# Kernel tuning notes

Measured on AMD Instinct MI355X. Metric: run time of the kernel, lower is better.

## Reference

```python
import jax, jax.numpy as jnp
import numpy as np

N_NODES = 50000
N_EDGES = 800000
DIM_IN = 128
DIM_OUT = 64


def setup_inputs() -> dict:
    key = jax.random.key(0)
    k1, k2, k3, k4 = jax.random.split(key, 4)
    x = jax.random.normal(k1, (N_NODES, DIM_IN), dtype=jnp.float32)
    edge_index = jax.random.randint(k2, (2, N_EDGES), 0, N_NODES, dtype=jnp.int64)
    W = jax.random.normal(k3, (DIM_IN, DIM_OUT), dtype=jnp.float32) / np.sqrt(DIM_IN)
    b = jax.random.normal(k4, (DIM_OUT,), dtype=jnp.float32) * 0.01
    return {"x": x, "edge_index": edge_index, "W": W, "b": b}


def reference(x, edge_index, W, b):
    # Faithful PyG GCNConv: add self-loops, symmetric deg normalization,
    # linear transform then normalized scatter-add aggregation, then bias.
    N = x.shape[0]
    h = x @ W  # [N, dim_out] — transform before propagate (PyG order)

    loops = jnp.arange(N, dtype=edge_index.dtype)
    src = jnp.concatenate([edge_index[0], loops])  # [E+N]
    dst = jnp.concatenate([edge_index[1], loops])  # [E+N]

    ones = jnp.ones(src.shape[0], dtype=h.dtype)
    deg = jax.ops.segment_sum(ones, dst, num_segments=N)  # in-degree incl. self-loop
    dinv = jnp.where(deg > 0, jax.lax.rsqrt(deg), 0.0)
    norm = dinv[src] * dinv[dst]  # [E+N]

    msgs = h[src] * norm[:, None]  # gather + scale
    out = jax.ops.segment_sum(msgs, dst, num_segments=N) + b  # scatter-add
    return jax.nn.log_softmax(out, axis=1)
```

## Files before the change

### kernel.cpp

```cpp
#include <hip/hip_runtime.h>
#include <hip/hip_fp16.h>
#include <cstdint>
#include <cstddef>

#define N_NODES 50000
#define N_EDGES 800000
#define DIM_IN  128
#define DIM_OUT 64

#define BSHIFT  6
#define BNODES  64
#define NB      1024
#define NBK     ((N_NODES + BNODES - 1) / BNODES)
#define EB      4096
#define SORTB   ((N_EDGES + EB - 1) / EB)
#define NE4     (N_EDGES / 4)
#define CAPB    1280
#define GROWS   512
#define GEMMB   ((N_NODES + GROWS - 1) / GROWS)
#define GPAD    16

typedef _Float16 f16x8 __attribute__((ext_vector_type(8)));
typedef float    f32x4 __attribute__((ext_vector_type(4)));

__global__ __launch_bounds__(256) void k_zero(int* __restrict__ gcnt) {
    const int i = blockIdx.x * 256 + threadIdx.x;
    if (i < NB * GPAD) gcnt[i] = 0;
}

__global__ __launch_bounds__(1024) void kFG(const int* __restrict__ ei,
                                            int* __restrict__ gcnt,
                                            unsigned* __restrict__ pairs,
                                            const float* __restrict__ x,
                                            const float* __restrict__ W,
                                            __half* __restrict__ h) {
    const int t = threadIdx.x;
    if (blockIdx.x < SORTB) {
        __shared__ int hcnt[NB];
        __shared__ int cur[NB];
        const int blk = blockIdx.x;
        hcnt[t] = 0;
        __syncthreads();
        const int4* src4 = (const int4*)ei;
        const int4* dst4 = (const int4*)(ei + N_EDGES);
        const int g = blk * (EB / 4) + t;
        int4 sv, dv;
        const bool live = (g < NE4);
        if (live) {
            dv = dst4[g];
            sv = src4[g];
            atomicAdd(&hcnt[dv.x >> BSHIFT], 1);
            atomicAdd(&hcnt[dv.y >> BSHIFT], 1);
            atomicAdd(&hcnt[dv.z >> BSHIFT], 1);
            atomicAdd(&hcnt[dv.w >> BSHIFT], 1);
        }
        __syncthreads();
        {
            const int c = hcnt[t];
            const int base = c ? atomicAdd(&gcnt[t * GPAD], c) : 0;
            cur[t] = t * CAPB + base;
        }
        __syncthreads();
        if (live) {
            int b, p;
            b = dv.x >> BSHIFT; p = atomicAdd(&cur[b], 1);
            if (p < b * CAPB + CAPB) pairs[p] = ((unsigned)sv.x << 16) | (unsigned)dv.x;
            b = dv.y >> BSHIFT; p = atomicAdd(&cur[b], 1);
            if (p < b * CAPB + CAPB) pairs[p] = ((unsigned)sv.y << 16) | (unsigned)dv.y;
            b = dv.z >> BSHIFT; p = atomicAdd(&cur[b], 1);
            if (p < b * CAPB + CAPB) pairs[p] = ((unsigned)sv.z << 16) | (unsigned)dv.z;
            b = dv.w >> BSHIFT; p = atomicAdd(&cur[b], 1);
            if (p < b * CAPB + CAPB) pairs[p] = ((unsigned)sv.w << 16) | (unsigned)dv.w;
        }
    } else {
        const int u = blockIdx.x - SORTB;
        const int w = t >> 6;
        const int l = t & 63;
        const int q = l >> 4;
        const int m16 = l & 15;

        f16x8 bf[4][4];
#pragma unroll
        for (int kc = 0; kc < 4; ++kc)
#pragma unroll
            for (int ct = 0; ct < 4; ++ct) {
                const float* wp = W + (size_t)(kc * 32 + q * 8) * DIM_OUT + ct * 16 + m16;
                f16x8 v;
#pragma unroll
                for (int j = 0; j < 8; ++j) v[j] = (_Float16)wp[(size_t)j * DIM_OUT];
                bf[kc][ct] = v;
            }

        const int base = u * GROWS + w * 32;
#pragma unroll
        for (int rt = 0; rt < 2; ++rt) {
            const int m0 = base + rt * 16;
            int mrow = m0 + m16;
            if (mrow >= N_NODES) mrow = N_NODES - 1;

            f16x8 af[4];
#pragma unroll
            for (int kc = 0; kc < 4; ++kc) {
                const float4* xp = (const float4*)(x + (size_t)mrow * DIM_IN + kc * 32 + q * 8);
                const float4 p0 = xp[0], p1 = xp[1];
                f16x8 a;
                a[0] = (_Float16)p0.x; a[1] = (_Float16)p0.y;
                a[2] = (_Float16)p0.z; a[3] = (_Float16)p0.w;
                a[4] = (_Float16)p1.x; a[5] = (_Float16)p1.y;
                a[6] = (_Float16)p1.z; a[7] = (_Float16)p1.w;
                af[kc] = a;
            }

            f32x4 acc[4];
#pragma unroll
            for (int ct = 0; ct < 4; ++ct) acc[ct] = (f32x4){0.f, 0.f, 0.f, 0.f};
#pragma unroll
            for (int kc = 0; kc < 4; ++kc)
#pragma unroll
                for (int ct = 0; ct < 4; ++ct)
                    acc[ct] = __builtin_amdgcn_mfma_f32_16x16x32_f16(af[kc], bf[kc][ct], acc[ct], 0, 0, 0);

#pragma unroll
            for (int reg = 0; reg < 4; ++reg) {
                const int r = m0 + q * 4 + reg;
                if (r < N_NODES) {
#pragma unroll
                    for (int ct = 0; ct < 4; ++ct)
                        h[(size_t)r * DIM_OUT + ct * 16 + m16] = __float2half(acc[ct][reg]);
                }
            }
        }
    }
}

__global__ __launch_bounds__(256) void kScale(const unsigned* __restrict__ pairs,
                                              const int* __restrict__ gcnt,
                                              __half* __restrict__ h) {
    __shared__ int cnt[BNODES];
    __shared__ float sdinv[BNODES];
    const int b = blockIdx.x, t = threadIdx.x;
    const int eb = b * CAPB;
    const int count = min(gcnt[b * GPAD], CAPB);
    const int ee = eb + count;

    if (t < BNODES) cnt[t] = 0;
    __syncthreads();

    {
        int i = eb + t;
        for (; i + 768 < ee; i += 1024) {
            const unsigned p0 = pairs[i];
            const unsigned p1 = pairs[i + 256];
            const unsigned p2 = pairs[i + 512];
            const unsigned p3 = pairs[i + 768];
            atomicAdd(&cnt[p0 & (BNODES - 1)], 1);
            atomicAdd(&cnt[p1 & (BNODES - 1)], 1);
            atomicAdd(&cnt[p2 & (BNODES - 1)], 1);
            atomicAdd(&cnt[p3 & (BNODES - 1)], 1);
        }
        for (; i < ee; i += 256) atomicAdd(&cnt[pairs[i] & (BNODES - 1)], 1);
    }
    __syncthreads();

    if (t < BNODES) sdinv[t] = rsqrtf((float)(cnt[t] + 1));
    __syncthreads();

    f16x8* h8w = (f16x8*)h;
    for (int idx = t; idx < BNODES * 8; idx += 256) {
        const int r = idx >> 3;
        const int n = (b << BSHIFT) + r;
        if (n < N_NODES) {
            const float d = sdinv[r];
            f16x8 v = h8w[(size_t)n * 8 + (idx & 7)];
#pragma unroll
            for (int j = 0; j < 8; ++j) v[j] = (_Float16)((float)v[j] * d);
            h8w[(size_t)n * 8 + (idx & 7)] = v;
        }
    }
}

__global__ __launch_bounds__(512) void kAgg(const unsigned* __restrict__ pairs,
                                            const int* __restrict__ gcnt,
                                            const __half* __restrict__ h,
                                            const float* __restrict__ bvec,
                                            float* __restrict__ out) {
    __shared__ int cnt[BNODES];
    __shared__ int cur[BNODES];
    __shared__ float sdinv[BNODES];
    __shared__ unsigned short lcsr[CAPB];
    const int b = blockIdx.x, t = threadIdx.x;
    const int eb = b * CAPB;
    const int count = min(gcnt[b * GPAD], CAPB);
    const int ee = eb + count;

    if (t < BNODES) cnt[t] = 0;
    __syncthreads();

    {
        int i = eb + t;
        for (; i + 512 < ee; i += 1024) {
            const unsigned p0 = pairs[i];
            const unsigned p1 = pairs[i + 512];
            atomicAdd(&cnt[p0 & (BNODES - 1)], 1);
            atomicAdd(&cnt[p1 & (BNODES - 1)], 1);
        }
        for (; i < ee; i += 512) atomicAdd(&cnt[pairs[i] & (BNODES - 1)], 1);
    }
    __syncthreads();

    if (t < 64) {
        const int lane = t;
        const int v = cnt[lane];
        int xs = v;
#pragma unroll
        for (int off = 1; off < 64; off <<= 1) {
            int y = __shfl_up(xs, off);
            if (lane >= off) xs += y;
        }
        cur[lane] = xs - v;
        sdinv[lane] = rsqrtf((float)(v + 1));
    }
    __syncthreads();

    for (int i = eb + t; i < ee; i += 512) {
        const unsigned p = pairs[i];
        const int q = atomicAdd(&cur[p & (BNODES - 1)], 1);
        lcsr[q] = (unsigned short)(p >> 16);
    }
    __syncthreads();

    const int r = t >> 3, sl = t & 7;
    const int n = (b << BSHIFT) + r;
    if (n >= N_NODES) return;
    const f16x8* __restrict__ h8 = (const f16x8*)h;

    const int s1 = cur[r];
    const int s0 = s1 - cnt[r];
    const float di = sdinv[r];

    const f16x8 hv = h8[(size_t)n * 8 + sl];
    float a[8];
#pragma unroll
    for (int j = 0; j < 8; ++j) a[j] = (float)hv[j];

    int i = s0;
    for (; i + 4 <= s1; i += 4) {
        const int c0 = lcsr[i + 0];
        const int c1 = lcsr[i + 1];
        const int c2 = lcsr[i + 2];
        const int c3 = lcsr[i + 3];
        const f16x8 v0 = h8[(size_t)c0 * 8 + sl];
        const f16x8 v1 = h8[(size_t)c1 * 8 + sl];
        const f16x8 v2 = h8[(size_t)c2 * 8 + sl];
        const f16x8 v3 = h8[(size_t)c3 * 8 + sl];
#pragma unroll
        for (int j = 0; j < 8; ++j)
            a[j] += (float)v0[j] + (float)v1[j] + (float)v2[j] + (float)v3[j];
    }
    for (; i < s1; ++i) {
        const f16x8 v0 = h8[(size_t)lcsr[i] * 8 + sl];
#pragma unroll
        for (int j = 0; j < 8; ++j) a[j] += (float)v0[j];
    }

    const float4 b0 = *(const float4*)&bvec[8 * sl];
    const float4 b1 = *(const float4*)&bvec[8 * sl + 4];
    float v[8];
    v[0] = a[0] * di + b0.x; v[1] = a[1] * di + b0.y;
    v[2] = a[2] * di + b0.z; v[3] = a[3] * di + b0.w;
    v[4] = a[4] * di + b1.x; v[5] = a[5] * di + b1.y;
    v[6] = a[6] * di + b1.z; v[7] = a[7] * di + b1.w;

    float m = v[0];
#pragma unroll
    for (int j = 1; j < 8; ++j) m = fmaxf(m, v[j]);
#pragma unroll
    for (int o = 4; o > 0; o >>= 1) m = fmaxf(m, __shfl_xor(m, o));
    float s = 0.f;
#pragma unroll
    for (int j = 0; j < 8; ++j) s += __expf(v[j] - m);
#pragma unroll
    for (int o = 4; o > 0; o >>= 1) s += __shfl_xor(s, o);
    const float ls = m + __logf(s);

    float4 o0, o1;
    o0.x = v[0] - ls; o0.y = v[1] - ls; o0.z = v[2] - ls; o0.w = v[3] - ls;
    o1.x = v[4] - ls; o1.y = v[5] - ls; o1.z = v[6] - ls; o1.w = v[7] - ls;
    *(float4*)&out[(size_t)n * DIM_OUT + 8 * sl]     = o0;
    *(float4*)&out[(size_t)n * DIM_OUT + 8 * sl + 4] = o1;
}

extern "C" void kernel_launch(void* const* d_in, const int* in_sizes, int n_in,
                              void* d_out, int out_size, void* d_ws, size_t ws_size,
                              hipStream_t stream) {
    const float* x  = (const float*)d_in[0];
    const int*   ei = (const int*)d_in[1];
    const float* W  = (const float*)d_in[2];
    const float* b  = (const float*)d_in[3];
    float* out = (float*)d_out;

    char* ws = (char*)d_ws;
    __half*   h     = (__half*)ws;   ws += (size_t)N_NODES * DIM_OUT * sizeof(__half);
    unsigned* pairs = (unsigned*)ws; ws += (size_t)NB * CAPB * sizeof(unsigned);
    int*      gcnt  = (int*)ws;      ws += (size_t)NB * GPAD * sizeof(int);

    k_zero <<<(NB * GPAD + 255) / 256, 256, 0, stream>>>(gcnt);
    kFG    <<<SORTB + GEMMB, 1024, 0, stream>>>(ei, gcnt, pairs, x, W, h);
    kScale <<<NBK, 256, 0, stream>>>(pairs, gcnt, h);
    kAgg   <<<NBK, 512, 0, stream>>>(pairs, gcnt, h, b, out);
}
```

Baseline: 124.5 us.

## Coarsen bucket sort to 256-node buckets and split sort from gather

Buckets of 256 destination nodes replace 64-node buckets, so the sort phase runs far fewer blocks and fewer global counter atomics. A new kSort kernel counts per-node degrees, builds a per-bucket CSR written to global memory with per-node offsets, and applies the dinv scaling to h in the same pass. A separate gather kernel with small 32-node blocks then reads the CSR for better load balance and occupancy. In exchange the CSR makes an extra round trip through global memory, and the larger bucket capacity raises the risk of overflowing when degrees are skewed.

Result: faster. 121.5 us (-2.4%).

```diff
diff --git a/kernel.cpp b/kernel.cpp
--- a/kernel.cpp
+++ b/kernel.cpp
@@ -8,24 +8,24 @@
 #define DIM_IN  128
 #define DIM_OUT 64
 
-#define BSHIFT  6
-#define BNODES  64
-#define NB      1024
-#define NBK     ((N_NODES + BNODES - 1) / BNODES)
+#define B2SHIFT 8
+#define B2NODES 256
+#define NB2     ((N_NODES + B2NODES - 1) / B2NODES)
 #define EB      4096
 #define SORTB   ((N_EDGES + EB - 1) / EB)
 #define NE4     (N_EDGES / 4)
-#define CAPB    1280
+#define CAPB    4864
 #define GROWS   512
 #define GEMMB   ((N_NODES + GROWS - 1) / GROWS)
 #define GPAD    16
+#define NEGRP   ((N_NODES + 31) / 32)
 
 typedef _Float16 f16x8 __attribute__((ext_vector_type(8)));
 typedef float    f32x4 __attribute__((ext_vector_type(4)));
 
 __global__ __launch_bounds__(256) void k_zero(int* __restrict__ gcnt) {
     const int i = blockIdx.x * 256 + threadIdx.x;
-    if (i < NB * GPAD) gcnt[i] = 0;
+    if (i < NB2 * GPAD) gcnt[i] = 0;
 }
 
 __global__ __launch_bounds__(1024) void kFG(const int* __restrict__ ei,
@@ -36,10 +36,10 @@
                                             __half* __restrict__ h) {
     const int t = threadIdx.x;
     if (blockIdx.x < SORTB) {
-        __shared__ int hcnt[NB];
-        __shared__ int cur[NB];
+        __shared__ int hcnt[B2NODES];
+        __shared__ int cur[B2NODES];
         const int blk = blockIdx.x;
-        hcnt[t] = 0;
+        if (t < B2NODES) hcnt[t] = 0;
         __syncthreads();
         const int4* src4 = (const int4*)ei;
         const int4* dst4 = (const int4*)(ei + N_EDGES);
@@ -49,13 +49,13 @@
         if (live) {
             dv = dst4[g];
             sv = src4[g];
-            atomicAdd(&hcnt[dv.x >> BSHIFT], 1);
-            atomicAdd(&hcnt[dv.y >> BSHIFT], 1);
-            atomicAdd(&hcnt[dv.z >> BSHIFT], 1);
-            atomicAdd(&hcnt[dv.w >> BSHIFT], 1);
+            atomicAdd(&hcnt[dv.x >> B2SHIFT], 1);
+            atomicAdd(&hcnt[dv.y >> B2SHIFT], 1);
+            atomicAdd(&hcnt[dv.z >> B2SHIFT], 1);
+            atomicAdd(&hcnt[dv.w >> B2SHIFT], 1);
         }
         __syncthreads();
-        {
+        if (t < NB2) {
             const int c = hcnt[t];
             const int base = c ? atomicAdd(&gcnt[t * GPAD], c) : 0;
             cur[t] = t * CAPB + base;
@@ -63,13 +63,13 @@
         __syncthreads();
         if (live) {
             int b, p;
-            b = dv.x >> BSHIFT; p = atomicAdd(&cur[b], 1);
+            b = dv.x >> B2SHIFT; p = atomicAdd(&cur[b], 1);
             if (p < b * CAPB + CAPB) pairs[p] = ((unsigned)sv.x << 16) | (unsigned)dv.x;
-            b = dv.y >> BSHIFT; p = atomicAdd(&cur[b], 1);
+            b = dv.y >> B2SHIFT; p = atomicAdd(&cur[b], 1);
             if (p < b * CAPB + CAPB) pairs[p] = ((unsigned)sv.y << 16) | (unsigned)dv.y;
-            b = dv.z >> BSHIFT; p = atomicAdd(&cur[b], 1);
+            b = dv.z >> B2SHIFT; p = atomicAdd(&cur[b], 1);
             if (p < b * CAPB + CAPB) pairs[p] = ((unsigned)sv.z << 16) | (unsigned)dv.z;
-            b = dv.w >> BSHIFT; p = atomicAdd(&cur[b], 1);
+            b = dv.w >> B2SHIFT; p = atomicAdd(&cur[b], 1);
             if (p < b * CAPB + CAPB) pairs[p] = ((unsigned)sv.w << 16) | (unsigned)dv.w;
         }
     } else {
@@ -133,110 +133,111 @@
     }
 }
 
-__global__ __launch_bounds__(256) void kScale(const unsigned* __restrict__ pairs,
-                                              const int* __restrict__ gcnt,
-                                              __half* __restrict__ h) {
-    __shared__ int cnt[BNODES];
-    __shared__ float sdinv[BNODES];
-    const int b = blockIdx.x, t = threadIdx.x;
-    const int eb = b * CAPB;
-    const int count = min(gcnt[b * GPAD], CAPB);
-    const int ee = eb + count;
-
-    if (t < BNODES) cnt[t] = 0;
-    __syncthreads();
-
-    {
-        int i = eb + t;
-        for (; i + 768 < ee; i += 1024) {
-            const unsigned p0 = pairs[i];
-            const unsigned p1 = pairs[i + 256];
-            const unsigned p2 = pairs[i + 512];
-            const unsigned p3 = pairs[i + 768];
-            atomicAdd(&cnt[p0 & (BNODES - 1)], 1);
-            atomicAdd(&cnt[p1 & (BNODES - 1)], 1);
-            atomicAdd(&cnt[p2 & (BNODES - 1)], 1);
-            atomicAdd(&cnt[p3 & (BNODES - 1)], 1);
-        }
-        for (; i < ee; i += 256) atomicAdd(&cnt[pairs[i] & (BNODES - 1)], 1);
-    }
-    __syncthreads();
-
-    if (t < BNODES) sdinv[t] = rsqrtf((float)(cnt[t] + 1));
-    __syncthreads();
-
-    f16x8* h8w = (f16x8*)h;
-    for (int idx = t; idx < BNODES * 8; idx += 256) {
-        const int r = idx >> 3;
-        const int n = (b << BSHIFT) + r;
-        if (n < N_NODES) {
-            const float d = sdinv[r];
-            f16x8 v = h8w[(size_t)n * 8 + (idx & 7)];
-#pragma unroll
-            for (int j = 0; j < 8; ++j) v[j] = (_Float16)((float)v[j] * d);
-            h8w[(size_t)n * 8 + (idx & 7)] = v;
-        }
-    }
-}
-
-__global__ __launch_bounds__(512) void kAgg(const unsigned* __restrict__ pairs,
-                                            const int* __restrict__ gcnt,
-                                            const __half* __restrict__ h,
-                                            const float* __restrict__ bvec,
-                                            float* __restrict__ out) {
-    __shared__ int cnt[BNODES];
-    __shared__ int cur[BNODES];
-    __shared__ float sdinv[BNODES];
+__global__ __launch_bounds__(512) void kSort(const unsigned* __restrict__ pairs,
+                                             const int* __restrict__ gcnt,
+                                             unsigned short* __restrict__ csr,
+                                             int2* __restrict__ nodeoff2,
+                                             __half* __restrict__ h) {
+    __shared__ int cnt[B2NODES];
+    __shared__ int cur[B2NODES];
+    __shared__ float sdinv[B2NODES];
+    __shared__ int wsum[4];
     __shared__ unsigned short lcsr[CAPB];
     const int b = blockIdx.x, t = threadIdx.x;
     const int eb = b * CAPB;
     const int count = min(gcnt[b * GPAD], CAPB);
     const int ee = eb + count;
 
-    if (t < BNODES) cnt[t] = 0;
+    if (t < B2NODES) cnt[t] = 0;
     __syncthreads();
 
     {
         int i = eb + t;
-        for (; i + 512 < ee; i += 1024) {
+        for (; i + 1536 < ee; i += 2048) {
             const unsigned p0 = pairs[i];
             const unsigned p1 = pairs[i + 512];
-            atomicAdd(&cnt[p0 & (BNODES - 1)], 1);
-            atomicAdd(&cnt[p1 & (BNODES - 1)], 1);
-        }
-        for (; i < ee; i += 512) atomicAdd(&cnt[pairs[i] & (BNODES - 1)], 1);
-    }
-    __syncthreads();
-
-    if (t < 64) {
-        const int lane = t;
-        const int v = cnt[lane];
+            const unsigned p2 = pairs[i + 1024];
+            const unsigned p3 = pairs[i + 1536];
+            atomicAdd(&cnt[p0 & (B2NODES - 1)], 1);
+            atomicAdd(&cnt[p1 & (B2NODES - 1)], 1);
+            atomicAdd(&cnt[p2 & (B2NODES - 1)], 1);
+            atomicAdd(&cnt[p3 & (B2NODES - 1)], 1);
+        }
+        for (; i < ee; i += 512) atomicAdd(&cnt[pairs[i] & (B2NODES - 1)], 1);
+    }
+    __syncthreads();
+
+    if (t < B2NODES) {
+        const int lane = t & 63;
+        const int v = cnt[t];
         int xs = v;
 #pragma unroll
         for (int off = 1; off < 64; off <<= 1) {
             int y = __shfl_up(xs, off);
             if (lane >= off) xs += y;
         }
-        cur[lane] = xs - v;
-        sdinv[lane] = rsqrtf((float)(v + 1));
+        cur[t] = xs;
+        if (lane == 63) wsum[t >> 6] = xs;
+    }
+    __syncthreads();
+    if (t == 0) {
+        int acc = 0;
+#pragma unroll
+        for (int w2 = 0; w2 < 4; ++w2) { const int v2 = wsum[w2]; wsum[w2] = acc; acc += v2; }
+    }
+    __syncthreads();
+    if (t < B2NODES) {
+        const int v = cnt[t];
+        const int excl = cur[t] - v + wsum[t >> 6];
+        sdinv[t] = rsqrtf((float)(v + 1));
+        const int n = (b << B2SHIFT) + t;
+        if (n < N_NODES) nodeoff2[n] = make_int2(eb + excl, v);
+        cur[t] = excl;
     }
     __syncthreads();
 
     for (int i = eb + t; i < ee; i += 512) {
         const unsigned p = pairs[i];
-        const int q = atomicAdd(&cur[p & (BNODES - 1)], 1);
+        const int q = atomicAdd(&cur[p & (B2NODES - 1)], 1);
         lcsr[q] = (unsigned short)(p >> 16);
     }
     __syncthreads();
 
-    const int r = t >> 3, sl = t & 7;
-    const int n = (b << BSHIFT) + r;
+    {
+        const int cw = (count + 1) >> 1;
+        const unsigned* l32 = (const unsigned*)lcsr;
+        unsigned* c32 = (unsigned*)(csr + eb);
+        for (int i2 = t; i2 < cw; i2 += 512) c32[i2] = l32[i2];
+    }
+    {
+        f16x8* h8w = (f16x8*)h;
+        for (int idx = t; idx < B2NODES * 8; idx += 512) {
+            const int r = idx >> 3;
+            const int n = (b << B2SHIFT) + r;
+            if (n < N_NODES) {
+                const float d = sdinv[r];
+                f16x8 v = h8w[(size_t)n * 8 + (idx & 7)];
+#pragma unroll
+                for (int j = 0; j < 8; ++j) v[j] = (_Float16)((float)v[j] * d);
+                h8w[(size_t)n * 8 + (idx & 7)] = v;
+            }
+        }
+    }
+}
+
+__global__ __launch_bounds__(256) void kE_agg(const int2* __restrict__ nodeoff2,
+                                              const unsigned short* __restrict__ csr,
+                                              const __half* __restrict__ h,
+                                              const float* __restrict__ bvec,
+                                              float* __restrict__ out) {
+    const int t = threadIdx.x;
+    const int ew = t >> 3, sl = t & 7;
+    const int n = blockIdx.x * 32 + ew;
     if (n >= N_NODES) return;
     const f16x8* __restrict__ h8 = (const f16x8*)h;
 
-    const int s1 = cur[r];
-    const int s0 = s1 - cnt[r];
-    const float di = sdinv[r];
+    const int2 off = nodeoff2[n];
+    const int s0 = off.x, s1 = off.x + off.y;
 
     const f16x8 hv = h8[(size_t)n * 8 + sl];
     float a[8];
@@ -245,10 +246,10 @@
 
     int i = s0;
     for (; i + 4 <= s1; i += 4) {
-        const int c0 = lcsr[i + 0];
-        const int c1 = lcsr[i + 1];
-        const int c2 = lcsr[i + 2];
-        const int c3 = lcsr[i + 3];
+        const int c0 = csr[i + 0];
+        const int c1 = csr[i + 1];
+        const int c2 = csr[i + 2];
+        const int c3 = csr[i + 3];
         const f16x8 v0 = h8[(size_t)c0 * 8 + sl];
         const f16x8 v1 = h8[(size_t)c1 * 8 + sl];
         const f16x8 v2 = h8[(size_t)c2 * 8 + sl];
@@ -258,13 +259,14 @@
             a[j] += (float)v0[j] + (float)v1[j] + (float)v2[j] + (float)v3[j];
     }
     for (; i < s1; ++i) {
-        const f16x8 v0 = h8[(size_t)lcsr[i] * 8 + sl];
+        const f16x8 v0 = h8[(size_t)csr[i] * 8 + sl];
 #pragma unroll
         for (int j = 0; j < 8; ++j) a[j] += (float)v0[j];
     }
 
     const float4 b0 = *(const float4*)&bvec[8 * sl];
     const float4 b1 = *(const float4*)&bvec[8 * sl + 4];
+    const float di = rsqrtf((float)(off.y + 1));
     float v[8];
     v[0] = a[0] * di + b0.x; v[1] = a[1] * di + b0.y;
     v[2] = a[2] * di + b0.z; v[3] = a[3] * di + b0.w;
@@ -300,12 +302,14 @@
     float* out = (float*)d_out;
 
     char* ws = (char*)d_ws;
-    __half*   h     = (__half*)ws;   ws += (size_t)N_NODES * DIM_OUT * sizeof(__half);
-    unsigned* pairs = (unsigned*)ws; ws += (size_t)NB * CAPB * sizeof(unsigned);
-    int*      gcnt  = (int*)ws;      ws += (size_t)NB * GPAD * sizeof(int);
-
-    k_zero <<<(NB * GPAD + 255) / 256, 256, 0, stream>>>(gcnt);
+    __half*         h        = (__half*)ws;         ws += (size_t)N_NODES * DIM_OUT * sizeof(__half);
+    unsigned*       pairs    = (unsigned*)ws;       ws += (size_t)NB2 * CAPB * sizeof(unsigned);
+    unsigned short* csr      = (unsigned short*)ws; ws += (size_t)NB2 * CAPB * sizeof(unsigned short);
+    int2*           nodeoff2 = (int2*)ws;           ws += (size_t)N_NODES * sizeof(int2);
+    int*            gcnt     = (int*)ws;            ws += (size_t)NB2 * GPAD * sizeof(int);
+
+    k_zero <<<(NB2 * GPAD + 255) / 256, 256, 0, stream>>>(gcnt);
     kFG    <<<SORTB + GEMMB, 1024, 0, stream>>>(ei, gcnt, pairs, x, W, h);
-    kScale <<<NBK, 256, 0, stream>>>(pairs, gcnt, h);
-    kAgg   <<<NBK, 512, 0, stream>>>(pairs, gcnt, h, b, out);
-}
+    kSort  <<<NB2, 512, 0, stream>>>(pairs, gcnt, csr, nodeoff2, h);
+    kE_agg <<<NEGRP, 256, 0, stream>>>(nodeoff2, csr, h, b, out);
+}
```
